# Kernel tuning notes

Measured on AMD Instinct MI355X. Metric: run time of the kernel, lower is better.

## Reference

```python
import jax, jax.numpy as jnp
import numpy as np

K = 5                      # spline kernel_size per dim
NEG = -1e30                # finite -inf stand-in for max-scatter init
_COMBO = np.indices((2, 2, 2)).reshape(3, 8).T   # [8,3] corner offsets of the deg-1 B-spline support
_STRIDE = np.array([1, K, K * K])


def spline_basis(pseudo):
    # pseudo: [E,3] in [0,1]; open degree-1 B-spline, kernel_size K per dim.
    v = jnp.clip(pseudo, 0.0, 1.0) * (K - 1)
    i0 = jnp.clip(jnp.floor(v), 0, K - 2)
    f = v - i0                                   # [E,3] fractional part
    c = jnp.asarray(_COMBO)                      # [8,3]
    w = jnp.prod(jnp.where(c[None] == 1, f[:, None, :], 1.0 - f[:, None, :]), axis=2)  # [E,8]
    k = jnp.sum((i0.astype(jnp.int32)[:, None, :] + c[None]) * jnp.asarray(_STRIDE)[None, None, :], axis=2)  # [E,8]
    return w, k


def spline_conv(x, src, dst, pseudo, W, root, bias):
    # x:[N,Fin], W:[K^3,Fin,Fout]. Gather-spline-scatter, mean aggregation + root weight + bias.
    N = x.shape[0]
    U = jnp.einsum('ni,kio->nko', x, W)          # [N,K^3,Fout] all-kernel transform (dense GEMM)
    bw, kidx = spline_basis(pseudo)              # [E,8], [E,8]
    msg = jnp.sum(bw[:, :, None] * U[src[:, None], kidx], axis=1)  # [E,Fout]
    deg = jnp.zeros((N,), x.dtype).at[dst].add(1.0)
    agg = jnp.zeros((N, W.shape[2]), x.dtype).at[dst].add(msg) / jnp.maximum(deg, 1.0)[:, None]
    return agg + x @ root + bias


def weighted_max_pool(x, w, cluster, C):
    # keep features of the max-attention-weight node in each voxel cluster
    seg_w = jnp.full((C,), NEG, x.dtype).at[cluster].max(w)
    winner = w >= seg_w[cluster]
    pooled = jnp.full((C, x.shape[1]), NEG, x.dtype).at[cluster].max(jnp.where(winner[:, None], x, NEG))
    return jnp.where(pooled <= NEG / 2, 0.0, pooled)


def dense_max_pool(x, cluster, C):
    pooled = jnp.full((C, x.shape[1]), NEG, x.dtype).at[cluster].max(x)
    return jnp.where(pooled <= NEG / 2, 0.0, pooled)


def setup_inputs() -> dict:
    key = jax.random.key(0)
    ks = iter(jax.random.split(key, 80))
    N = [30000, 10000, 4000, 1500, 600]
    E = [360000, 120000, 48000, 18000, 7200]
    Fin = [1, 32, 64, 64, 64]
    Fout = [32, 64, 64, 64, 64]
    Cs = [10000, 4000, 1500, 600, 128]
    d = {"x": jax.random.normal(next(ks), (N[0], 1), jnp.float32)}
    for l in range(5):
        d[f"src{l}"] = jax.random.randint(next(ks), (E[l],), 0, N[l], jnp.int32)
        d[f"dst{l}"] = jax.random.randint(next(ks), (E[l],), 0, N[l], jnp.int32)
        d[f"pseudo{l}"] = jax.random.uniform(next(ks), (E[l], 3), jnp.float32)
    for l in range(5):
        d[f"cluster{l+1}"] = jax.random.randint(next(ks), (N[l],), 0, Cs[l], jnp.int32)
    for l in range(5):
        d[f"W{l+1}"] = 0.1 * jax.random.normal(next(ks), (K ** 3, Fin[l], Fout[l]), jnp.float32)
        d[f"root{l+1}"] = 0.1 * jax.random.normal(next(ks), (Fin[l], Fout[l]), jnp.float32)
        d[f"b{l+1}"] = jnp.zeros((Fout[l],), jnp.float32)
    for l, fdim in enumerate([32, 64, 64, 64]):
        d[f"attw{l+1}"] = 0.1 * jax.random.normal(next(ks), (fdim, 2), jnp.float32)
        d[f"attb{l+1}"] = jnp.zeros((2,), jnp.float32)
    d["fcw"] = 0.05 * jax.random.normal(next(ks), (512, 10), jnp.float32)
    d["fcb"] = jnp.zeros((10,), jnp.float32)
    return d


def reference(x, src0, dst0, pseudo0, src1, dst1, pseudo1, src2, dst2, pseudo2,
              src3, dst3, pseudo3, src4, dst4, pseudo4,
              cluster1, cluster2, cluster3, cluster4, cluster5,
              W1, root1, b1, W2, root2, b2, W3, root3, b3, W4, root4, b4, W5, root5, b5,
              attw1, attb1, attw2, attb2, attw3, attb3, attw4, attb4, fcw, fcb):
    h = jax.nn.elu(spline_conv(x, src0, dst0, pseudo0, W1, root1, b1))
    h = weighted_max_pool(h, (h @ attw1 + attb1)[:, 0], cluster1, 10000)
    h = jax.nn.elu(spline_conv(h, src1, dst1, pseudo1, W2, root2, b2))
    h = weighted_max_pool(h, (h @ attw2 + attb2)[:, 0], cluster2, 4000)
    h = jax.nn.elu(spline_conv(h, src2, dst2, pseudo2, W3, root3, b3))
    h = weighted_max_pool(h, (h @ attw3 + attb3)[:, 0], cluster3, 1500)
    h = jax.nn.elu(spline_conv(h, src3, dst3, pseudo3, W4, root4, b4))
    h = weighted_max_pool(h, (h @ attw4 + attb4)[:, 0], cluster4, 600)
    h = jax.nn.relu(spline_conv(h, src4, dst4, pseudo4, W5, root5, b5))
    h = dense_max_pool(h, cluster5, 128)        # [128, 64] = 16 graphs x 8 voxels
    z = h.reshape(-1, 512)                      # [16, 8*64]
    return jax.nn.log_softmax(z @ fcw + fcb, axis=1)
```

## Files before the change

kernel.cpp:

```cpp
#include <hip/hip_runtime.h>
#include <math.h>

#define KS 5
#define NEGV (-1e30f)

typedef __bf16 bf16x8 __attribute__((ext_vector_type(8)));
typedef float f32x4 __attribute__((ext_vector_type(4)));

__device__ __forceinline__ unsigned int flipf(float f) {
    unsigned int b = __float_as_uint(f);
    return b ^ ((b >> 31) ? 0xFFFFFFFFu : 0x80000000u);
}
__device__ __forceinline__ float unflipf(unsigned int u) {
    unsigned int b = u ^ ((u >> 31) ? 0x80000000u : 0xFFFFFFFFu);
    return __uint_as_float(b);
}
__device__ __forceinline__ float pread(unsigned int u) {
    return (u == 0u) ? 0.f : unflipf(u);
}

__device__ __forceinline__ void basis1(float p, int& b, float& f) {
    float v = fminf(fmaxf(p, 0.f), 1.f) * (float)(KS - 1);
    float fl = fminf(floorf(v), (float)(KS - 2));
    b = (int)fl; f = v - fl;
}

__device__ const int cE[5]     = {360000, 120000, 48000, 18000, 7200};
__device__ const int cN[5]     = {30000, 10000, 4000, 1500, 600};
__device__ const int cNB[5]    = {512, 469, 188, 71, 29};
__device__ const int cStart[5] = {0, 512, 981, 1169, 1240};
__device__ const int cBTend[5] = {8192, 139264, 401408, 663552, 925696};
__device__ const int cLFIN[5]  = {0, 5, 6, 6, 6};
__device__ const int cLFOUT[5] = {5, 6, 6, 6, 6};
__device__ const int cLKB[5]   = {2, 5, 6, 6, 6};

#define PREP_BLOCKS 1269
#define BPACK_TOT   925696

struct BatchPtrs {
    const float* ps[5];
    const int*   dst[5];
    int*   cell[5];
    int*   ctrl[5];
    int*   blkbase[5];
    float* deg[5];
    float* rankf[5];
    int*   dstbase[5];
    int*   eord[5];
};

struct BpackPtrs {
    const float* W[5];
    __bf16* H[5];
    __bf16* M[5];
    __bf16* L[5];
};

__global__ void edge_prep_all(BatchPtrs P)
{
    __shared__ int lh[64];
    int b = blockIdx.x;
    int l = (b >= 512) + (b >= 981) + (b >= 1169) + (b >= 1240);
    int lb = b - cStart[l];
    int E = cE[l];
    int stride = cNB[l] * 256;
    const float* pseudo = P.ps[l];
    const int* dst = P.dst[l];
    int* cell = P.cell[l];
    float* deg = P.deg[l];
    float* rankf = P.rankf[l];

    int t = threadIdx.x;
    if (t < 64) lh[t] = 0;
    __syncthreads();
    for (int e = lb * 256 + t; e < E; e += stride) {
        int b0, b1, b2; float f0, f1, f2;
        basis1(pseudo[e * 3 + 0], b0, f0);
        basis1(pseudo[e * 3 + 1], b1, f1);
        basis1(pseudo[e * 3 + 2], b2, f2);
        int c = b0 + 4 * b1 + 16 * b2;
        cell[e] = c;
        atomicAdd(&lh[c], 1);
        rankf[e] = atomicAdd(&deg[dst[e]], 1.0f);
    }
    __syncthreads();
    if (t < 64) P.blkbase[l][lb * 64 + t] = atomicAdd(&P.ctrl[l][t], lh[t]);
}

__global__ void scan5(BatchPtrs P)
{
    __shared__ int wexc[16];
    __shared__ int tot;
    __shared__ int carry;
    int l = blockIdx.x;
    int* ctrl = P.ctrl[l];
    const float* deg = P.deg[l];
    int* dstbase = P.dstbase[l];
    int N = cN[l];

    int t = (int)threadIdx.x;
    int lane = t & 63;
    int wid = t >> 6;
    if (t == 0) carry = 0;
    if (t < 64) {
        int h = ctrl[t];
        int x = h;
        #pragma unroll
        for (int off = 1; off < 64; off <<= 1) {
            int y = __shfl_up(x, off, 64);
            if (lane >= off) x += y;
        }
        int excl = x - h;
        ctrl[128 + t] = excl;
        int ch = (h + 63) >> 6;
        int cx = ch;
        #pragma unroll
        for (int off = 1; off < 64; off <<= 1) {
            int y = __shfl_up(cx, off, 64);
            if (lane >= off) cx += y;
        }
        ctrl[200 + t] = cx - ch;
        if (t == 63) {
            ctrl[128 + 64] = excl + h;
            ctrl[200 + 64] = cx;
            ctrl[272] = cx;
        }
    }
    __syncthreads();
    for (int base = 0; base < N; base += 4096) {
        int i0 = base + t * 4;
        int4 v = make_int4(0, 0, 0, 0);
        if (i0 < N) {
            float4 d = *reinterpret_cast<const float4*>(deg + i0);
            v.x = (int)d.x; v.y = (int)d.y; v.z = (int)d.z; v.w = (int)d.w;
        }
        int s = v.x + v.y + v.z + v.w;
        int x = s;
        #pragma unroll
        for (int off = 1; off < 64; off <<= 1) {
            int y = __shfl_up(x, off, 64);
            if (lane >= off) x += y;
        }
        if (lane == 63) wexc[wid] = x;
        __syncthreads();
        if (t < 16) {
            int a = wexc[t];
            int inc = a;
            #pragma unroll
            for (int off = 1; off < 16; off <<= 1) {
                int y = __shfl_up(inc, off, 16);
                if (t >= off) inc += y;
            }
            wexc[t] = inc - a;
            if (t == 15) tot = inc;
        }
        __syncthreads();
        if (i0 < N) {
            int e0 = carry + wexc[wid] + (x - s);
            int4 o;
            o.x = e0;
            o.y = e0 + v.x;
            o.z = o.y + v.y;
            o.w = o.z + v.z;
            *reinterpret_cast<int4*>(dstbase + i0) = o;
        }
        __syncthreads();
        if (t == 0) carry += tot;
        __syncthreads();
    }
    if (t == 0) dstbase[N] = carry;
}

__global__ void edge_scatter_all(BatchPtrs P)
{
    __shared__ int cur[64];
    int b = blockIdx.x;
    int l = (b >= 512) + (b >= 981) + (b >= 1169) + (b >= 1240);
    int lb = b - cStart[l];
    int E = cE[l];
    int stride = cNB[l] * 256;
    const int* cell = P.cell[l];
    const int* dst = P.dst[l];
    const int* dstbase = P.dstbase[l];
    float* rankf = P.rankf[l];
    int* posb = (int*)rankf;
    int* eord = P.eord[l];

    int t = threadIdx.x;
    if (t < 64) cur[t] = P.ctrl[l][128 + t] + P.blkbase[l][lb * 64 + t];
    __syncthreads();
    for (int e = lb * 256 + t; e < E; e += stride) {
        int p = atomicAdd(&cur[cell[e]], 1);
        eord[p] = e;
        int r = (int)rankf[e];
        posb[e] = dstbase[dst[e]] + r;
    }
}

__global__ void bpack_all(BpackPtrs B)
{
    int t = blockIdx.x * blockDim.x + threadIdx.x;
    if (t >= BPACK_TOT) return;
    int l = (t >= 8192) + (t >= 139264) + (t >= 401408) + (t >= 663552);
    int tl = t - (l ? cBTend[l - 1] : 0);
    int lfout = cLFOUT[l], lkb = cLKB[l], lfin = cLFIN[l];
    int fin = 1 << lfin;
    const float* W = B.W[l];
    int o = tl & ((1 << lfout) - 1);
    int kb = (tl >> lfout) & ((1 << lkb) - 1);
    int cellid = tl >> (lfout + lkb);
    int b0 = cellid & 3, b1 = (cellid >> 2) & 3, b2 = cellid >> 4;
    bf16x8 vh, vm, vl;
    #pragma unroll
    for (int j = 0; j < 8; ++j) {
        int r = kb * 8 + j;
        float val = 0.f;
        if (r < (fin << 3)) {
            int c = r >> lfin;
            int i = r & (fin - 1);
            int k = (b0 + (c & 1)) + 5 * (b1 + ((c >> 1) & 1)) + 25 * (b2 + (c >> 2));
            val = W[((((size_t)k << lfin) + i) << lfout) + o];
        }
        __bf16 hv = (__bf16)val;
        vh[j] = hv;
        float r1 = val - (float)hv;
        __bf16 mv = (__bf16)r1;
        vm[j] = mv;
        vl[j] = (__bf16)(r1 - (float)mv);
    }
    *reinterpret_cast<bf16x8*>(B.H[l] + (size_t)tl * 8) = vh;
    *reinterpret_cast<bf16x8*>(B.M[l] + (size_t)tl * 8) = vm;
    *reinterpret_cast<bf16x8*>(B.L[l] + (size_t)tl * 8) = vl;
}

template<int FIN, int FOUT, bool FLIPIN>
__global__ void conv_mfma(const void* __restrict__ xin,
                          const int* __restrict__ src,
                          const float* __restrict__ pseudo,
                          const __bf16* __restrict__ BpH,
                          const __bf16* __restrict__ BpM,
                          const __bf16* __restrict__ BpL,
                          const int* __restrict__ ctrl,
                          const int* __restrict__ eord,
                          const int* __restrict__ posb,
                          float* __restrict__ msg)
{
    constexpr int KB = (FIN == 1) ? 4 : FIN;
    constexpr int KSTEPS = (FIN == 1) ? 1 : FIN / 4;
    constexpr int NF = FOUT / 16;
    constexpr int SLICE = 4 * FOUT * 8;

    __shared__ float cst[64][FOUT + 1];
    __shared__ int posv[64];
    __shared__ __bf16 bsh[3][SLICE];

    int bid = blockIdx.x;
    if (bid >= ctrl[272]) return;
    int blo = 0, bhi = 64;
    while (blo + 1 < bhi) {
        int mid = (blo + bhi) >> 1;
        if (ctrl[200 + mid] <= bid) blo = mid; else bhi = mid;
    }
    int bucket = blo;
    int m0 = (bid - ctrl[200 + bucket]) << 6;
    int bbase = ctrl[128 + bucket];
    int bsize = ctrl[128 + bucket + 1] - bbase;

    int tt = threadIdx.x;
    int lane = tt & 63;
    int wave = tt >> 6;
    int h4 = lane >> 4;
    int col = lane & 15;
    int row = m0 + wave * 16 + col;
    bool valid = row < bsize;
    int e = eord[bbase + (valid ? row : 0)];
    int s = src[e];

    if (tt < 64) {
        int orow = m0 + tt;
        posv[tt] = (orow < bsize) ? posb[eord[bbase + orow]] : -1;
    }

    float bw[8];
    {
        int b0, b1, b2; float f0, f1, f2;
        basis1(pseudo[e * 3 + 0], b0, f0);
        basis1(pseudo[e * 3 + 1], b1, f1);
        basis1(pseudo[e * 3 + 2], b2, f2);
        float g0 = 1.f - f0, g1 = 1.f - f1, g2 = 1.f - f2;
        float vf = valid ? 1.f : 0.f;
        #pragma unroll
        for (int j = 0; j < 8; ++j)
            bw[j] = vf * ((j & 1) ? f0 : g0) * (((j >> 1) & 1) ? f1 : g1) * (((j >> 2) & 1) ? f2 : g2);
    }

    float xv[8], xw[8];
    float xsc = 0.f;
    #pragma unroll
    for (int j = 0; j < 8; ++j) { xv[j] = 0.f; xw[j] = 0.f; }
    if (FIN >= 32) {
        if (FLIPIN) {
            const uint4* xb = reinterpret_cast<const uint4*>((const unsigned int*)xin + (size_t)s * FIN + h4 * 8);
            uint4 u0 = xb[0], u1 = xb[1];
            xv[0] = pread(u0.x); xv[1] = pread(u0.y); xv[2] = pread(u0.z); xv[3] = pread(u0.w);
            xv[4] = pread(u1.x); xv[5] = pread(u1.y); xv[6] = pread(u1.z); xv[7] = pread(u1.w);
            if (FIN == 64) {
                const uint4* xb2 = reinterpret_cast<const uint4*>((const unsigned int*)xin + (size_t)s * FIN + 32 + h4 * 8);
                uint4 w0 = xb2[0], w1 = xb2[1];
                xw[0] = pread(w0.x); xw[1] = pread(w0.y); xw[2] = pread(w0.z); xw[3] = pread(w0.w);
                xw[4] = pread(w1.x); xw[5] = pread(w1.y); xw[6] = pread(w1.z); xw[7] = pread(w1.w);
            }
        } else {
            const float4* xb = reinterpret_cast<const float4*>((const float*)xin + (size_t)s * FIN + h4 * 8);
            float4 u0 = xb[0], u1 = xb[1];
            xv[0] = u0.x; xv[1] = u0.y; xv[2] = u0.z; xv[3] = u0.w;
            xv[4] = u1.x; xv[5] = u1.y; xv[6] = u1.z; xv[7] = u1.w;
            if (FIN == 64) {
                const float4* xb2 = reinterpret_cast<const float4*>((const float*)xin + (size_t)s * FIN + 32 + h4 * 8);
                float4 w0 = xb2[0], w1 = xb2[1];
                xw[0] = w0.x; xw[1] = w0.y; xw[2] = w0.z; xw[3] = w0.w;
                xw[4] = w1.x; xw[5] = w1.y; xw[6] = w1.z; xw[7] = w1.w;
            }
        }
    } else {
        xsc = ((const float*)xin)[s];
    }

    f32x4 acc[NF];
    #pragma unroll
    for (int nf = 0; nf < NF; ++nf) acc[nf] = (f32x4){0.f, 0.f, 0.f, 0.f};

    for (int kt = 0; kt < KSTEPS; ++kt) {
        __syncthreads();
        {
            size_t gbase = ((size_t)bucket * KB + kt * 4) * FOUT * 8;
            int idx = tt * 8;
            if (idx < SLICE) {
                *reinterpret_cast<bf16x8*>(&bsh[0][idx]) =
                    *reinterpret_cast<const bf16x8*>(BpH + gbase + idx);
                *reinterpret_cast<bf16x8*>(&bsh[1][idx]) =
                    *reinterpret_cast<const bf16x8*>(BpM + gbase + idx);
                *reinterpret_cast<bf16x8*>(&bsh[2][idx]) =
                    *reinterpret_cast<const bf16x8*>(BpL + gbase + idx);
            }
        }
        __syncthreads();

        float v[8];
        if (FIN == 64) {
            float bwc = bw[kt >> 1];
            const float* u = (kt & 1) ? xw : xv;
            #pragma unroll
            for (int j = 0; j < 8; ++j) v[j] = u[j] * bwc;
        } else if (FIN == 32) {
            float bwc = bw[kt];
            #pragma unroll
            for (int j = 0; j < 8; ++j) v[j] = xv[j] * bwc;
        } else {
            float xm = (h4 == 0) ? xsc : 0.f;
            #pragma unroll
            for (int j = 0; j < 8; ++j) v[j] = bw[j] * xm;
        }
        bf16x8 ah, am, al;
        #pragma unroll
        for (int j = 0; j < 8; ++j) {
            __bf16 hv = (__bf16)v[j];
            ah[j] = hv;
            float r1 = v[j] - (float)hv;
            __bf16 mv = (__bf16)r1;
            am[j] = mv;
            al[j] = (__bf16)(r1 - (float)mv);
        }
        #pragma unroll
        for (int nf = 0; nf < NF; ++nf) {
            int loff = (h4 * FOUT + nf * 16 + col) * 8;
            bf16x8 bh = *reinterpret_cast<const bf16x8*>(&bsh[0][loff]);
            bf16x8 bm = *reinterpret_cast<const bf16x8*>(&bsh[1][loff]);
            bf16x8 bl = *reinterpret_cast<const bf16x8*>(&bsh[2][loff]);
            acc[nf] = __builtin_amdgcn_mfma_f32_16x16x32_bf16(ah, bh, acc[nf], 0, 0, 0);
            acc[nf] = __builtin_amdgcn_mfma_f32_16x16x32_bf16(ah, bm, acc[nf], 0, 0, 0);
            acc[nf] = __builtin_amdgcn_mfma_f32_16x16x32_bf16(am, bh, acc[nf], 0, 0, 0);
            acc[nf] = __builtin_amdgcn_mfma_f32_16x16x32_bf16(am, bm, acc[nf], 0, 0, 0);
            acc[nf] = __builtin_amdgcn_mfma_f32_16x16x32_bf16(ah, bl, acc[nf], 0, 0, 0);
            acc[nf] = __builtin_amdgcn_mfma_f32_16x16x32_bf16(al, bh, acc[nf], 0, 0, 0);
        }
    }

    #pragma unroll
    for (int nf = 0; nf < NF; ++nf)
        #pragma unroll
        for (int j = 0; j < 4; ++j)
            cst[wave * 16 + h4 * 4 + j][nf * 16 + col] = acc[nf][j];
    __syncthreads();

    constexpr int F4 = FOUT / 4;
    constexpr int ITER = 64 * F4 / 256;
    #pragma unroll
    for (int i = 0; i < ITER; ++i) {
        int idx = i * 256 + tt;
        int r = idx / F4;
        int c4 = idx - r * F4;
        int p = posv[r];
        if (p >= 0) {
            float4 vq = make_float4(cst[r][c4 * 4], cst[r][c4 * 4 + 1],
                                    cst[r][c4 * 4 + 2], cst[r][c4 * 4 + 3]);
            *reinterpret_cast<float4*>(msg + (size_t)p * FOUT + c4 * 4) = vq;
        }
    }
}

template<int FIN, int FOUT, int ACT, int POOLMODE, bool FLIPIN>
__global__ void node_finalize(const void* __restrict__ xin,
                              const float* __restrict__ msg,
                              const int* __restrict__ dstbase,
                              const float* __restrict__ deg,
                              const float* __restrict__ root,
                              const float* __restrict__ bias,
                              const float* __restrict__ attw,
                              const float* __restrict__ attb,
                              const int* __restrict__ cluster,
                              float* __restrict__ out,
                              float* __restrict__ wbuf,
                              unsigned int* __restrict__ segw,
                              unsigned int* __restrict__ pooled,
                              int N)
{
    int t = blockIdx.x * blockDim.x + threadIdx.x;
    int n = t / FOUT, o = t % FOUT;
    if (n >= N) return;
    int b0 = dstbase[n];
    int dn = (int)deg[n];
    float a = 0.f;
    for (int r = 0; r < dn; ++r)
        a += msg[(size_t)(b0 + r) * FOUT + o];
    a = a / fmaxf((float)dn, 1.f) + bias[o];
    #pragma unroll
    for (int i = 0; i < FIN; ++i) {
        float xi;
        if (FLIPIN) xi = pread(((const unsigned int*)xin)[(size_t)n * FIN + i]);
        else        xi = ((const float*)xin)[(size_t)n * FIN + i];
        a = fmaf(xi, root[i * FOUT + o], a);
    }
    if (ACT == 0) a = (a > 0.f) ? a : expm1f(a);
    else          a = fmaxf(a, 0.f);
    if (POOLMODE == 1) {
        atomicMax(&pooled[(size_t)cluster[n] * FOUT + o], flipf(a));
        return;
    }
    out[t] = a;
    float w = a * attw[2 * o];
    #pragma unroll
    for (int off = FOUT / 2; off >= 1; off >>= 1)
        w += __shfl_xor(w, off, 64);
    if (o == 0) {
        float wt = w + attb[0];
        wbuf[n] = wt;
        atomicMax(&segw[cluster[n]], flipf(wt));
    }
}

template<int F>
__global__ void pool_scatter(const float* __restrict__ x,
                             const float* __restrict__ wout,
                             const unsigned int* __restrict__ segw,
                             const int* __restrict__ cluster,
                             unsigned int* __restrict__ pooled, int N)
{
    int gs = gridDim.x * blockDim.x;
    int total = N * F;
    for (int t = blockIdx.x * blockDim.x + threadIdx.x; t < total; t += gs) {
        int n = t / F;
        int f = t - n * F;
        int c = cluster[n];
        if (wout[n] >= unflipf(segw[c]))
            atomicMax(&pooled[(size_t)c * F + f], flipf(x[t]));
    }
}

__global__ void pool_final_fc(const unsigned int* __restrict__ pooled,
                              const float* __restrict__ fcw,
                              const float* __restrict__ fcb,
                              float* __restrict__ out)
{
    __shared__ float h[8192];
    __shared__ float logits[16][10];
    __shared__ float lse[16];
    int t = threadIdx.x;
    for (int i = t; i < 8192; i += 512)
        h[i] = pread(pooled[i]);
    __syncthreads();
    if (t < 160) {
        int g = t / 10, cls = t - g * 10;
        float a = fcb[cls];
        for (int j = 0; j < 512; ++j)
            a = fmaf(h[g * 512 + j], fcw[j * 10 + cls], a);
        logits[g][cls] = a;
    }
    __syncthreads();
    if (t < 16) {
        float m = -1e30f;
        for (int c = 0; c < 10; ++c) m = fmaxf(m, logits[t][c]);
        float s = 0.f;
        for (int c = 0; c < 10; ++c) s += expf(logits[t][c] - m);
        lse[t] = m + logf(s);
    }
    __syncthreads();
    if (t < 160) out[t] = logits[t / 10][t - (t / 10) * 10] - lse[t / 10];
}

static inline int igrid(long long total, int block, int cap = 2048) {
    long long g = (total + block - 1) / block;
    if (g > cap) g = cap;
    if (g < 1) g = 1;
    return (int)g;
}

static const int hE[5] = {360000, 120000, 48000, 18000, 7200};
static const int hN[5] = {30000, 10000, 4000, 1500, 600};
static const int hC[5] = {10000, 4000, 1500, 600, 128};

#define OFF_HA     0
#define OFF_HB     960000
#define OFF_DEG    1280000
#define OFF_CTRL   1326112
#define OFF_SEGW   1328672
#define OFF_POOL   1344912
#define ZERO_FLTS  783504
#define OFF_BLK    2063504
#define OFF_DSTB   2144720
#define OFF_CELL   2190896
#define OFF_RANK   2744112
#define OFF_EORD   3297328
#define OFF_BP     3850544
#define OFF_MSG    14958896
#define OFF_WBUF   26478896

static const int cumN_h[5]    = {0, 30000, 40000, 44000, 45500};
static const int cumC_h[5]    = {0, 10000, 14000, 15500, 16100};
static const int cumCF_h[5]   = {0, 320000, 576000, 672000, 710400};
static const int cumBLK_h[5]  = {0, 32768, 62784, 74816, 79360};
static const int cumDSTB_h[5] = {0, 30016, 40032, 44048, 45568};
static const int cumE_h[5]    = {0, 360000, 480000, 528000, 546000};
static const size_t planeB_h[5] = {65536, 1048576, 2097152, 2097152, 2097152};
static const size_t cumBPf_h[5] = {0, 98304, 1671168, 4816896, 7962624};

extern "C" void kernel_launch(void* const* d_in, const int* in_sizes, int n_in,
                              void* d_out, int out_size, void* d_ws, size_t ws_size,
                              hipStream_t stream)
{
    const float* x0 = (const float*)d_in[0];
    const int*   src_[5]  = {(const int*)d_in[1], (const int*)d_in[4], (const int*)d_in[7], (const int*)d_in[10], (const int*)d_in[13]};
    const int*   dst_[5]  = {(const int*)d_in[2], (const int*)d_in[5], (const int*)d_in[8], (const int*)d_in[11], (const int*)d_in[14]};
    const float* ps_[5]   = {(const float*)d_in[3], (const float*)d_in[6], (const float*)d_in[9], (const float*)d_in[12], (const float*)d_in[15]};
    const int*   cl_[5]   = {(const int*)d_in[16], (const int*)d_in[17], (const int*)d_in[18], (const int*)d_in[19], (const int*)d_in[20]};
    const float* W_[5]    = {(const float*)d_in[21], (const float*)d_in[24], (const float*)d_in[27], (const float*)d_in[30], (const float*)d_in[33]};
    const float* root_[5] = {(const float*)d_in[22], (const float*)d_in[25], (const float*)d_in[28], (const float*)d_in[31], (const float*)d_in[34]};
    const float* b_[5]    = {(const float*)d_in[23], (const float*)d_in[26], (const float*)d_in[29], (const float*)d_in[32], (const float*)d_in[35]};
    const float* attw_[4] = {(const float*)d_in[36], (const float*)d_in[38], (const float*)d_in[40], (const float*)d_in[42]};
    const float* attb_[4] = {(const float*)d_in[37], (const float*)d_in[39], (const float*)d_in[41], (const float*)d_in[43]};
    const float* fcw = (const float*)d_in[44];
    const float* fcb = (const float*)d_in[45];

    float* ws_f = (float*)d_ws;
    float* hA = ws_f + OFF_HA;
    float* wbuf = ws_f + OFF_WBUF;
    float* msg = ws_f + OFF_MSG;

    BatchPtrs P;
    BpackPtrs BP;
    const __bf16* BpH_l[5]; const __bf16* BpM_l[5]; const __bf16* BpL_l[5];
    int* ctrl_l[5]; int* dstb_l[5]; int* eord_l[5]; int* posb_l[5];
    float* deg_l[5];
    unsigned int* segw_l[5]; unsigned int* pool_l[5];
    for (int l = 0; l < 5; ++l) {
        P.ps[l] = ps_[l];
        P.dst[l] = dst_[l];
        P.cell[l] = (int*)(ws_f + OFF_CELL + cumE_h[l]);
        P.ctrl[l] = (int*)(ws_f + OFF_CTRL + l * 512);
        P.blkbase[l] = (int*)(ws_f + OFF_BLK + cumBLK_h[l]);
        P.deg[l] = ws_f + OFF_DEG + cumN_h[l];
        P.rankf[l] = ws_f + OFF_RANK + cumE_h[l];
        P.dstbase[l] = (int*)(ws_f + OFF_DSTB + cumDSTB_h[l]);
        P.eord[l] = (int*)(ws_f + OFF_EORD + cumE_h[l]);
        __bf16* H = (__bf16*)(ws_f + OFF_BP + cumBPf_h[l]);
        BP.W[l] = W_[l];
        BP.H[l] = H;
        BP.M[l] = H + planeB_h[l];
        BP.L[l] = H + 2 * planeB_h[l];
        BpH_l[l] = BP.H[l]; BpM_l[l] = BP.M[l]; BpL_l[l] = BP.L[l];
        ctrl_l[l] = P.ctrl[l];
        dstb_l[l] = P.dstbase[l];
        eord_l[l] = P.eord[l];
        posb_l[l] = (int*)P.rankf[l];
        deg_l[l] = P.deg[l];
        segw_l[l] = (unsigned int*)(ws_f + OFF_SEGW + cumC_h[l]);
        pool_l[l] = (unsigned int*)(ws_f + OFF_POOL + cumCF_h[l]);
    }

    (void)hipMemsetAsync(ws_f + OFF_DEG, 0, (size_t)ZERO_FLTS * 4, stream);
    edge_prep_all<<<PREP_BLOCKS, 256, 0, stream>>>(P);
    scan5<<<5, 1024, 0, stream>>>(P);
    edge_scatter_all<<<PREP_BLOCKS, 256, 0, stream>>>(P);
    bpack_all<<<(BPACK_TOT + 255) / 256, 256, 0, stream>>>(BP);

    conv_mfma<1, 32, false><<<hE[0] / 64 + 65, 256, 0, stream>>>(
        x0, src_[0], ps_[0], BpH_l[0], BpM_l[0], BpL_l[0], ctrl_l[0], eord_l[0], posb_l[0], msg);
    node_finalize<1, 32, 0, 0, false><<<(hN[0] * 32) / 256, 256, 0, stream>>>(
        x0, msg, dstb_l[0], deg_l[0], root_[0], b_[0], attw_[0], attb_[0], cl_[0], hA, wbuf, segw_l[0], nullptr, hN[0]);
    pool_scatter<32><<<igrid((long long)hN[0] * 32, 256), 256, 0, stream>>>(
        hA, wbuf, segw_l[0], cl_[0], pool_l[0], hN[0]);

    conv_mfma<32, 64, true><<<hE[1] / 64 + 65, 256, 0, stream>>>(
        pool_l[0], src_[1], ps_[1], BpH_l[1], BpM_l[1], BpL_l[1], ctrl_l[1], eord_l[1], posb_l[1], msg);
    node_finalize<32, 64, 0, 0, true><<<(hN[1] * 64) / 256, 256, 0, stream>>>(
        pool_l[0], msg, dstb_l[1], deg_l[1], root_[1], b_[1], attw_[1], attb_[1], cl_[1], hA, wbuf, segw_l[1], nullptr, hN[1]);
    pool_scatter<64><<<igrid((long long)hN[1] * 64, 256), 256, 0, stream>>>(
        hA, wbuf, segw_l[1], cl_[1], pool_l[1], hN[1]);

    conv_mfma<64, 64, true><<<hE[2] / 64 + 65, 256, 0, stream>>>(
        pool_l[1], src_[2], ps_[2], BpH_l[2], BpM_l[2], BpL_l[2], ctrl_l[2], eord_l[2], posb_l[2], msg);
    node_finalize<64, 64, 0, 0, true><<<(hN[2] * 64) / 256, 256, 0, stream>>>(
        pool_l[1], msg, dstb_l[2], deg_l[2], root_[2], b_[2], attw_[2], attb_[2], cl_[2], hA, wbuf, segw_l[2], nullptr, hN[2]);
    pool_scatter<64><<<igrid((long long)hN[2] * 64, 256), 256, 0, stream>>>(
        hA, wbuf, segw_l[2], cl_[2], pool_l[2], hN[2]);

    conv_mfma<64, 64, true><<<hE[3] / 64 + 65, 256, 0, stream>>>(
        pool_l[2], src_[3], ps_[3], BpH_l[3], BpM_l[3], BpL_l[3], ctrl_l[3], eord_l[3], posb_l[3], msg);
    node_finalize<64, 64, 0, 0, true><<<(hN[3] * 64) / 256, 256, 0, stream>>>(
        pool_l[2], msg, dstb_l[3], deg_l[3], root_[3], b_[3], attw_[3], attb_[3], cl_[3], hA, wbuf, segw_l[3], nullptr, hN[3]);
    pool_scatter<64><<<igrid((long long)hN[3] * 64, 256), 256, 0, stream>>>(
        hA, wbuf, segw_l[3], cl_[3], pool_l[3], hN[3]);

    conv_mfma<64, 64, true><<<hE[4] / 64 + 65, 256, 0, stream>>>(
        pool_l[3], src_[4], ps_[4], BpH_l[4], BpM_l[4], BpL_l[4], ctrl_l[4], eord_l[4], posb_l[4], msg);
    node_finalize<64, 64, 1, 1, true><<<(hN[4] * 64) / 256, 256, 0, stream>>>(
        pool_l[3], msg, dstb_l[4], deg_l[4], root_[4], b_[4], nullptr, nullptr, cl_[4], nullptr, nullptr, nullptr, pool_l[4], hN[4]);
    pool_final_fc<<<1, 512, 0, stream>>>(pool_l[4], fcw, fcb, (float*)d_out);
}
```

Before: 306.4 us.

## Replace pooled feature scatter with argmax-index selection via 64-bit atomicMax

Attention-weighted max pooling no longer materialises pooled feature arrays. Each node does a single 64-bit atomicMax of the key (flipped weight, node index) per cluster. The next layer's conv and finalize kernels then gather the winning node's row through that index, with empty clusters read as zeros. This removes the separate pool_scatter kernels, their per-feature atomics and the larger zeroing memset. In exchange it adds an extra indirection on each gather, and when weights tie it keeps a single node's features rather than the elementwise max over the tied nodes.

```diff
diff --git a/kernel.cpp b/kernel.cpp
--- a/kernel.cpp
+++ b/kernel.cpp
@@ -2,10 +2,10 @@
 #include <math.h>
 
 #define KS 5
-#define NEGV (-1e30f)
 
 typedef __bf16 bf16x8 __attribute__((ext_vector_type(8)));
 typedef float f32x4 __attribute__((ext_vector_type(4)));
+typedef unsigned long long u64;
 
 __device__ __forceinline__ unsigned int flipf(float f) {
     unsigned int b = __float_as_uint(f);
@@ -233,8 +233,9 @@
     *reinterpret_cast<bf16x8*>(B.L[l] + (size_t)tl * 8) = vl;
 }
 
-template<int FIN, int FOUT, bool FLIPIN>
-__global__ void conv_mfma(const void* __restrict__ xin,
+template<int FIN, int FOUT, bool GATHER>
+__global__ void conv_mfma(const float* __restrict__ xin,
+                          const u64* __restrict__ win,
                           const int* __restrict__ src,
                           const float* __restrict__ pseudo,
                           const __bf16* __restrict__ BpH,
@@ -294,36 +295,35 @@
             bw[j] = vf * ((j & 1) ? f0 : g0) * (((j >> 1) & 1) ? f1 : g1) * (((j >> 2) & 1) ? f2 : g2);
     }
 
+    const float* xrow;
+    bool xok = true;
+    if (GATHER) {
+        u64 wv = win[s];
+        xok = (wv != 0ull);
+        xrow = xin + (size_t)(unsigned int)(wv & 0xffffffffu) * FIN;
+    } else {
+        xrow = xin + (size_t)s * FIN;
+    }
+
     float xv[8], xw[8];
     float xsc = 0.f;
     #pragma unroll
     for (int j = 0; j < 8; ++j) { xv[j] = 0.f; xw[j] = 0.f; }
     if (FIN >= 32) {
-        if (FLIPIN) {
-            const uint4* xb = reinterpret_cast<const uint4*>((const unsigned int*)xin + (size_t)s * FIN + h4 * 8);
-            uint4 u0 = xb[0], u1 = xb[1];
-            xv[0] = pread(u0.x); xv[1] = pread(u0.y); xv[2] = pread(u0.z); xv[3] = pread(u0.w);
-            xv[4] = pread(u1.x); xv[5] = pread(u1.y); xv[6] = pread(u1.z); xv[7] = pread(u1.w);
-            if (FIN == 64) {
-                const uint4* xb2 = reinterpret_cast<const uint4*>((const unsigned int*)xin + (size_t)s * FIN + 32 + h4 * 8);
-                uint4 w0 = xb2[0], w1 = xb2[1];
-                xw[0] = pread(w0.x); xw[1] = pread(w0.y); xw[2] = pread(w0.z); xw[3] = pread(w0.w);
-                xw[4] = pread(w1.x); xw[5] = pread(w1.y); xw[6] = pread(w1.z); xw[7] = pread(w1.w);
-            }
-        } else {
-            const float4* xb = reinterpret_cast<const float4*>((const float*)xin + (size_t)s * FIN + h4 * 8);
+        if (xok) {
+            const float4* xb = reinterpret_cast<const float4*>(xrow + h4 * 8);
             float4 u0 = xb[0], u1 = xb[1];
             xv[0] = u0.x; xv[1] = u0.y; xv[2] = u0.z; xv[3] = u0.w;
             xv[4] = u1.x; xv[5] = u1.y; xv[6] = u1.z; xv[7] = u1.w;
             if (FIN == 64) {
-                const float4* xb2 = reinterpret_cast<const float4*>((const float*)xin + (size_t)s * FIN + 32 + h4 * 8);
+                const float4* xb2 = reinterpret_cast<const float4*>(xrow + 32 + h4 * 8);
                 float4 w0 = xb2[0], w1 = xb2[1];
                 xw[0] = w0.x; xw[1] = w0.y; xw[2] = w0.z; xw[3] = w0.w;
                 xw[4] = w1.x; xw[5] = w1.y; xw[6] = w1.z; xw[7] = w1.w;
             }
         }
     } else {
-        xsc = ((const float*)xin)[s];
+        xsc = xrow[0];
     }
 
     f32x4 acc[NF];
@@ -409,8 +409,9 @@
     }
 }
 
-template<int FIN, int FOUT, int ACT, int POOLMODE, bool FLIPIN>
-__global__ void node_finalize(const void* __restrict__ xin,
+template<int FIN, int FOUT, int ACT, int POOLMODE, bool GATHER>
+__global__ void node_finalize(const float* __restrict__ xin,
+                              const u64* __restrict__ winprev,
                               const float* __restrict__ msg,
                               const int* __restrict__ dstbase,
                               const float* __restrict__ deg,
@@ -420,8 +421,7 @@
                               const float* __restrict__ attb,
                               const int* __restrict__ cluster,
                               float* __restrict__ out,
-                              float* __restrict__ wbuf,
-                              unsigned int* __restrict__ segw,
+                              u64* __restrict__ seg64,
                               unsigned int* __restrict__ pooled,
                               int N)
 {
@@ -434,12 +434,20 @@
     for (int r = 0; r < dn; ++r)
         a += msg[(size_t)(b0 + r) * FOUT + o];
     a = a / fmaxf((float)dn, 1.f) + bias[o];
-    #pragma unroll
-    for (int i = 0; i < FIN; ++i) {
-        float xi;
-        if (FLIPIN) xi = pread(((const unsigned int*)xin)[(size_t)n * FIN + i]);
-        else        xi = ((const float*)xin)[(size_t)n * FIN + i];
-        a = fmaf(xi, root[i * FOUT + o], a);
+
+    const float* xrow;
+    bool xok = true;
+    if (GATHER) {
+        u64 wv = winprev[n];
+        xok = (wv != 0ull);
+        xrow = xin + (size_t)(unsigned int)(wv & 0xffffffffu) * FIN;
+    } else {
+        xrow = xin + (size_t)n * FIN;
+    }
+    if (xok) {
+        #pragma unroll
+        for (int i = 0; i < FIN; ++i)
+            a = fmaf(xrow[i], root[i * FOUT + o], a);
     }
     if (ACT == 0) a = (a > 0.f) ? a : expm1f(a);
     else          a = fmaxf(a, 0.f);
@@ -454,26 +462,8 @@
         w += __shfl_xor(w, off, 64);
     if (o == 0) {
         float wt = w + attb[0];
-        wbuf[n] = wt;
-        atomicMax(&segw[cluster[n]], flipf(wt));
-    }
-}
-
-template<int F>
-__global__ void pool_scatter(const float* __restrict__ x,
-                             const float* __restrict__ wout,
-                             const unsigned int* __restrict__ segw,
-                             const int* __restrict__ cluster,
-                             unsigned int* __restrict__ pooled, int N)
-{
-    int gs = gridDim.x * blockDim.x;
-    int total = N * F;
-    for (int t = blockIdx.x * blockDim.x + threadIdx.x; t < total; t += gs) {
-        int n = t / F;
-        int f = t - n * F;
-        int c = cluster[n];
-        if (wout[n] >= unflipf(segw[c]))
-            atomicMax(&pooled[(size_t)c * F + f], flipf(x[t]));
+        u64 key = ((u64)flipf(wt) << 32) | (unsigned int)n;
+        atomicMax(&seg64[cluster[n]], key);
     }
 }
 
@@ -508,36 +498,26 @@
     if (t < 160) out[t] = logits[t / 10][t - (t / 10) * 10] - lse[t / 10];
 }
 
-static inline int igrid(long long total, int block, int cap = 2048) {
-    long long g = (total + block - 1) / block;
-    if (g > cap) g = cap;
-    if (g < 1) g = 1;
-    return (int)g;
-}
-
 static const int hE[5] = {360000, 120000, 48000, 18000, 7200};
 static const int hN[5] = {30000, 10000, 4000, 1500, 600};
-static const int hC[5] = {10000, 4000, 1500, 600, 128};
 
 #define OFF_HA     0
 #define OFF_HB     960000
-#define OFF_DEG    1280000
-#define OFF_CTRL   1326112
-#define OFF_SEGW   1328672
-#define OFF_POOL   1344912
-#define ZERO_FLTS  783504
-#define OFF_BLK    2063504
-#define OFF_DSTB   2144720
-#define OFF_CELL   2190896
-#define OFF_RANK   2744112
-#define OFF_EORD   3297328
-#define OFF_BP     3850544
-#define OFF_MSG    14958896
-#define OFF_WBUF   26478896
+#define OFF_DEG    1600000
+#define OFF_CTRL   1646112
+#define OFF_SEG64  1648672
+#define OFF_POOL4  1680880
+#define ZERO_FLTS  89072
+#define OFF_BLK    1689072
+#define OFF_DSTB   1770288
+#define OFF_CELL   1816464
+#define OFF_RANK   2369680
+#define OFF_EORD   2922896
+#define OFF_BP     3476112
+#define OFF_MSG    14584464
 
 static const int cumN_h[5]    = {0, 30000, 40000, 44000, 45500};
 static const int cumC_h[5]    = {0, 10000, 14000, 15500, 16100};
-static const int cumCF_h[5]   = {0, 320000, 576000, 672000, 710400};
 static const int cumBLK_h[5]  = {0, 32768, 62784, 74816, 79360};
 static const int cumDSTB_h[5] = {0, 30016, 40032, 44048, 45568};
 static const int cumE_h[5]    = {0, 360000, 480000, 528000, 546000};
@@ -563,15 +543,16 @@
 
     float* ws_f = (float*)d_ws;
     float* hA = ws_f + OFF_HA;
-    float* wbuf = ws_f + OFF_WBUF;
+    float* hB = ws_f + OFF_HB;
     float* msg = ws_f + OFF_MSG;
+    unsigned int* pool4 = (unsigned int*)(ws_f + OFF_POOL4);
 
     BatchPtrs P;
     BpackPtrs BP;
     const __bf16* BpH_l[5]; const __bf16* BpM_l[5]; const __bf16* BpL_l[5];
     int* ctrl_l[5]; int* dstb_l[5]; int* eord_l[5]; int* posb_l[5];
     float* deg_l[5];
-    unsigned int* segw_l[5]; unsigned int* pool_l[5];
+    u64* seg64_l[5];
     for (int l = 0; l < 5; ++l) {
         P.ps[l] = ps_[l];
         P.dst[l] = dst_[l];
@@ -593,8 +574,7 @@
         eord_l[l] = P.eord[l];
         posb_l[l] = (int*)P.rankf[l];
         deg_l[l] = P.deg[l];
-        segw_l[l] = (unsigned int*)(ws_f + OFF_SEGW + cumC_h[l]);
-        pool_l[l] = (unsigned int*)(ws_f + OFF_POOL + cumCF_h[l]);
+        seg64_l[l] = (u64*)(ws_f + OFF_SEG64) + cumC_h[l];
     }
 
     (void)hipMemsetAsync(ws_f + OFF_DEG, 0, (size_t)ZERO_FLTS * 4, stream);
@@ -604,36 +584,28 @@
     bpack_all<<<(BPACK_TOT + 255) / 256, 256, 0, stream>>>(BP);
 
     conv_mfma<1, 32, false><<<hE[0] / 64 + 65, 256, 0, stream>>>(
-        x0, src_[0], ps_[0], BpH_l[0], BpM_l[0], BpL_l[0], ctrl_l[0], eord_l[0], posb_l[0], msg);
+        x0, nullptr, src_[0], ps_[0], BpH_l[0], BpM_l[0], BpL_l[0], ctrl_l[0], eord_l[0], posb_l[0], msg);
     node_finalize<1, 32, 0, 0, false><<<(hN[0] * 32) / 256, 256, 0, stream>>>(
-        x0, msg, dstb_l[0], deg_l[0], root_[0], b_[0], attw_[0], attb_[0], cl_[0], hA, wbuf, segw_l[0], nullptr, hN[0]);
-    pool_scatter<32><<<igrid((long long)hN[0] * 32, 256), 256, 0, stream>>>(
-        hA, wbuf, segw_l[0], cl_[0], pool_l[0], hN[0]);
+        x0, nullptr, msg, dstb_l[0], deg_l[0], root_[0], b_[0], attw_[0], attb_[0], cl_[0], hA, seg64_l[0], nullptr, hN[0]);
 
     conv_mfma<32, 64, true><<<hE[1] / 64 + 65, 256, 0, stream>>>(
-        pool_l[0], src_[1], ps_[1], BpH_l[1], BpM_l[1], BpL_l[1], ctrl_l[1], eord_l[1], posb_l[1], msg);
+        hA, seg64_l[0], src_[1], ps_[1], BpH_l[1], BpM_l[1], BpL_l[1], ctrl_l[1], eord_l[1], posb_l[1], msg);
     node_finalize<32, 64, 0, 0, true><<<(hN[1] * 64) / 256, 256, 0, stream>>>(
-        pool_l[0], msg, dstb_l[1], deg_l[1], root_[1], b_[1], attw_[1], attb_[1], cl_[1], hA, wbuf, segw_l[1], nullptr, hN[1]);
-    pool_scatter<64><<<igrid((long long)hN[1] * 64, 256), 256, 0, stream>>>(
-        hA, wbuf, segw_l[1], cl_[1], pool_l[1], hN[1]);
+        hA, seg64_l[0], msg, dstb_l[1], deg_l[1], root_[1], b_[1], attw_[1], attb_[1], cl_[1], hB, seg64_l[1], nullptr, hN[1]);
 
     conv_mfma<64, 64, true><<<hE[2] / 64 + 65, 256, 0, stream>>>(
-        pool_l[1], src_[2], ps_[2], BpH_l[2], BpM_l[2], BpL_l[2], ctrl_l[2], eord_l[2], posb_l[2], msg);
+        hB, seg64_l[1], src_[2], ps_[2], BpH_l[2], BpM_l[2], BpL_l[2], ctrl_l[2], eord_l[2], posb_l[2], msg);
     node_finalize<64, 64, 0, 0, true><<<(hN[2] * 64) / 256, 256, 0, stream>>>(
-        pool_l[1], msg, dstb_l[2], deg_l[2], root_[2], b_[2], attw_[2], attb_[2], cl_[2], hA, wbuf, segw_l[2], nullptr, hN[2]);
-    pool_scatter<64><<<igrid((long long)hN[2] * 64, 256), 256, 0, stream>>>(
-        hA, wbuf, segw_l[2], cl_[2], pool_l[2], hN[2]);
+        hB, seg64_l[1], msg, dstb_l[2], deg_l[2], root_[2], b_[2], attw_[2], attb_[2], cl_[2], hA, seg64_l[2], nullptr, hN[2]);
 
     conv_mfma<64, 64, true><<<hE[3] / 64 + 65, 256, 0, stream>>>(
-        pool_l[2], src_[3], ps_[3], BpH_l[3], BpM_l[3], BpL_l[3], ctrl_l[3], eord_l[3], posb_l[3], msg);
+        hA, seg64_l[2], src_[3], ps_[3], BpH_l[3], BpM_l[3], BpL_l[3], ctrl_l[3], eord_l[3], posb_l[3], msg);
     node_finalize<64, 64, 0, 0, true><<<(hN[3] * 64) / 256, 256, 0, stream>>>(
-        pool_l[2], msg, dstb_l[3], deg_l[3], root_[3], b_[3], attw_[3], attb_[3], cl_[3], hA, wbuf, segw_l[3], nullptr, hN[3]);
-    pool_scatter<64><<<igrid((long long)hN[3] * 64, 256), 256, 0, stream>>>(
-        hA, wbuf, segw_l[3], cl_[3], pool_l[3], hN[3]);
+        hA, seg64_l[2], msg, dstb_l[3], deg_l[3], root_[3], b_[3], attw_[3], attb_[3], cl_[3], hB, seg64_l[3], nullptr, hN[3]);
 
     conv_mfma<64, 64, true><<<hE[4] / 64 + 65, 256, 0, stream>>>(
-        pool_l[3], src_[4], ps_[4], BpH_l[4], BpM_l[4], BpL_l[4], ctrl_l[4], eord_l[4], posb_l[4], msg);
+        hB, seg64_l[3], src_[4], ps_[4], BpH_l[4], BpM_l[4], BpL_l[4], ctrl_l[4], eord_l[4], posb_l[4], msg);
     node_finalize<64, 64, 1, 1, true><<<(hN[4] * 64) / 256, 256, 0, stream>>>(
-        pool_l[3], msg, dstb_l[4], deg_l[4], root_[4], b_[4], nullptr, nullptr, cl_[4], nullptr, nullptr, nullptr, pool_l[4], hN[4]);
-    pool_final_fc<<<1, 512, 0, stream>>>(pool_l[4], fcw, fcb, (float*)d_out);
-}
+        hB, seg64_l[3], msg, dstb_l[4], deg_l[4], root_[4], b_[4], nullptr, nullptr, cl_[4], nullptr, nullptr, pool4, hN[4]);
+    pool_final_fc<<<1, 512, 0, stream>>>(pool4, fcw, fcb, (float*)d_out);
+}
```

Measured after the change: 292.1 us. 4.7% less time.
